# Kernel optimization log

Measured on AMD Instinct MI355X. Metric: run time of the kernel, lower is better.

The kernel has to match this reference:

```python
import jax, jax.numpy as jnp
import numpy as np

N, NFEAT, NHID, NCLASS, H1 = 4096, 512, 64, 16, 8
GAIN = 1.414  # xavier gain used by the torch module
NEG_SLOPE = 0.2
MASK_VAL = -1e10


def _xavier(k, shape):
    fan_in, fan_out = shape[-2], shape[-1]
    lim = GAIN * (6.0 / (fan_in + fan_out)) ** 0.5
    return jax.random.uniform(k, shape, jnp.float32, -lim, lim)


def setup_inputs() -> dict:
    key = jax.random.key(0)
    ks = jax.random.split(key, 10)
    return {
        "x": jax.random.normal(ks[0], (N, NFEAT), jnp.float32),
        "adj": jax.random.randint(ks[1], (N, N), 0, 2, jnp.int32),
        # layer-1 parameters, stacked over H1 heads
        "W1": _xavier(ks[2], (H1, NFEAT, NHID)),
        "b1": jnp.zeros((H1, NHID), jnp.float32),
        "as1": _xavier(ks[3], (H1, NHID, 1))[..., 0],
        "an1": _xavier(ks[4], (H1, NHID, 1))[..., 0],
        # layer-2 parameters (single head, input = H1*NHID due to concat)
        "W2": _xavier(ks[5], (H1 * NHID, NCLASS)),
        "b2": jnp.zeros((NCLASS,), jnp.float32),
        "as2": _xavier(ks[6], (NCLASS, 1))[:, 0],
        "an2": _xavier(ks[7], (NCLASS, 1))[:, 0],
    }


def gat_layer(X, adj_pos, W, b, a_s, a_n):
    # X: [N, Fin], W: [Fin, Fout], a_s/a_n: [Fout], adj_pos: [N, N] bool
    feats = X @ W                                        # [N, Fout]
    s = feats @ a_s                                      # [N]
    nb = feats @ a_n                                     # [N]
    attn = jax.nn.leaky_relu(s[:, None] + nb[None, :], NEG_SLOPE)  # [N, N]
    attn = jnp.where(adj_pos, attn, MASK_VAL)
    attn = jax.nn.softmax(attn, axis=-1)
    # dropout on attn/feats is a no-op in eval mode
    return attn @ feats + b                              # [N, Fout]


def reference(x, adj, W1, b1, as1, an1, W2, b2, as2, an2):
    adj_pos = adj > 0
    # x dropout is a no-op in eval mode
    layer1 = jax.vmap(gat_layer, in_axes=(None, None, 0, 0, 0, 0))
    h = jax.nn.relu(layer1(x, adj_pos, W1, b1, as1, an1))    # [H1, N, NHID]
    h = jnp.transpose(h, (1, 0, 2)).reshape(N, H1 * NHID)    # concat heads on dim 1
    h = jax.nn.elu(h)
    out = jax.nn.relu(gat_layer(h, adj_pos, W2, b2, as2, an2))  # [N, NCLASS]
    return jax.nn.log_softmax(out, axis=1)
```

## Files before the change

### kernel.cpp

```cpp
#include <hip/hip_runtime.h>

#define NN 4096
#define NFEAT 512
#define NHID 64
#define H1 8
#define NCLS 16
#define BND 40.0f
#define VSTR 72

typedef short bf16x8 __attribute__((ext_vector_type(8)));
typedef float f32x4 __attribute__((ext_vector_type(4)));

__device__ __forceinline__ unsigned short f2bf(float f) {
    unsigned u = __float_as_uint(f);
    u += 0x7fffu + ((u >> 16) & 1u);
    return (unsigned short)(u >> 16);
}
__device__ __forceinline__ float leaky(float v) { return fmaxf(v, 0.2f * v); }
__device__ __forceinline__ unsigned pkbf(float lo, float hi) {
    return __builtin_amdgcn_perm(__float_as_uint(hi) + 0x8000u,
                                 __float_as_uint(lo) + 0x8000u, 0x07060302u);
}
__device__ __forceinline__ bf16x8 mk8(unsigned a, unsigned b, unsigned c, unsigned d) {
    union { unsigned u[4]; bf16x8 v; } cv;
    cv.u[0] = a; cv.u[1] = b; cv.u[2] = c; cv.u[3] = d; return cv.v;
}

__global__ __launch_bounds__(256)
void k_prep(const int* __restrict__ adj, unsigned long long* __restrict__ bits,
            const float* __restrict__ W1, unsigned short* __restrict__ w1f)
{
    __shared__ float wt[64][65];
    const int t = threadIdx.x, bx = blockIdx.x;
    if (bx < NN) {
        const int wv = t >> 6, lane = t & 63;
        const int* ap = adj + (size_t)bx * NN;
        for (int w = wv; w < 64; w += 4) {
            unsigned long long m = __ballot(ap[w * 64 + lane] > 0);
            if (lane == 0) bits[(size_t)bx * 64 + w] = m;
        }
        return;
    }
    const int kt = (bx - NN) & 7, h = (bx - NN) >> 3;
    #pragma unroll
    for (int i = 0; i < 4; ++i) {
        const int f = t + 256 * i;
        const int r = f >> 4, c4 = f & 15;
        const float4 v = *(const float4*)(W1 + ((size_t)(h * NFEAT) + kt * 64 + r) * NHID + c4 * 4);
        wt[r][c4 * 4 + 0] = v.x; wt[r][c4 * 4 + 1] = v.y;
        wt[r][c4 * 4 + 2] = v.z; wt[r][c4 * 4 + 3] = v.w;
    }
    __syncthreads();
    #pragma unroll
    for (int s = 0; s < 2; ++s) {
        const int o = t + s * 256;
        const int kg2 = o >> 8, rem = o & 255;
        const int nt = rem >> 6, lane2 = rem & 63;
        const int qq = lane2 >> 4, nn = lane2 & 15;
        const int kl = kg2 * 32 + qq * 8;
        const int c = nt * 16 + nn;
        uint4 w;
        w.x = pkbf(wt[kl + 0][c], wt[kl + 1][c]);
        w.y = pkbf(wt[kl + 2][c], wt[kl + 3][c]);
        w.z = pkbf(wt[kl + 4][c], wt[kl + 5][c]);
        w.w = pkbf(wt[kl + 6][c], wt[kl + 7][c]);
        *(uint4*)(w1f + (((size_t)h * 16 + kt * 2 + kg2) * 4 + nt) * 512 + lane2 * 8) = w;
    }
}

__global__ __launch_bounds__(256)
void k_feats1(const float* __restrict__ x, const unsigned short* __restrict__ w1f,
              const float* __restrict__ as1, const float* __restrict__ an1,
              unsigned short* __restrict__ f1bT, float* __restrict__ s1,
              float* __restrict__ F1a, float* __restrict__ F2a)
{
    const int t = threadIdx.x, wv = t >> 6, lane = t & 63;
    const int q = lane >> 4, n = lane & 15;
    const int h = blockIdx.y, R0 = blockIdx.x * 64;
    const int row = R0 + wv * 16 + n;
    const float* ap = x + (size_t)row * NFEAT;
    const unsigned short* wp = w1f + (size_t)h * 16 * 4 * 512 + lane * 8;
    f32x4 acc[4] = {{0.f,0.f,0.f,0.f},{0.f,0.f,0.f,0.f},{0.f,0.f,0.f,0.f},{0.f,0.f,0.f,0.f}};
    #pragma unroll 4
    for (int kg = 0; kg < 16; ++kg) {
        const float4 xa = *(const float4*)(ap + kg * 32 + q * 8);
        const float4 xb = *(const float4*)(ap + kg * 32 + q * 8 + 4);
        const bf16x8 af = mk8(pkbf(xa.x, xa.y), pkbf(xa.z, xa.w),
                              pkbf(xb.x, xb.y), pkbf(xb.z, xb.w));
        #pragma unroll
        for (int nt = 0; nt < 4; ++nt) {
            const bf16x8 bf = *(const bf16x8*)(wp + (size_t)(kg * 4 + nt) * 512);
            acc[nt] = __builtin_amdgcn_mfma_f32_16x16x32_bf16(af, bf, acc[nt], 0, 0, 0);
        }
    }
    #pragma unroll
    for (int nt = 0; nt < 4; ++nt) {
        uint2 w;
        w.x = pkbf(acc[nt][0], acc[nt][1]);
        w.y = pkbf(acc[nt][2], acc[nt][3]);
        *(uint2*)(f1bT + ((size_t)h * NHID + nt * 16 + n) * NN + R0 + wv * 16 + q * 4) = w;
    }
    float asv[4], anv[4];
    #pragma unroll
    for (int nt = 0; nt < 4; ++nt) {
        asv[nt] = as1[h * NHID + nt * 16 + n];
        anv[nt] = an1[h * NHID + nt * 16 + n];
    }
    #pragma unroll
    for (int i = 0; i < 4; ++i) {
        float ps = acc[0][i]*asv[0] + acc[1][i]*asv[1] + acc[2][i]*asv[2] + acc[3][i]*asv[3];
        float pn = acc[0][i]*anv[0] + acc[1][i]*anv[1] + acc[2][i]*anv[2] + acc[3][i]*anv[3];
        #pragma unroll
        for (int off = 8; off > 0; off >>= 1) {
            ps += __shfl_xor(ps, off, 64);
            pn += __shfl_xor(pn, off, 64);
        }
        if (n == 0) {
            const int idx = R0 + wv * 16 + q * 4 + i;
            s1[h * NN + idx] = ps;
            F1a[h * NN + idx] = __expf(pn - BND);
            F2a[h * NN + idx] = __expf(0.2f * (pn - BND));
        }
    }
}

__global__ __launch_bounds__(512, 4)
void k_gat1(const unsigned short* __restrict__ f1bT, const float* __restrict__ s1,
            const float* __restrict__ F1, const float* __restrict__ F2,
            const unsigned long long* __restrict__ abits, const float* __restrict__ b1,
            unsigned short* __restrict__ hcatb)
{
    __shared__ __align__(16) char smem[4 * 2 * 64 * VSTR * 2];
    unsigned short* vT = (unsigned short*)smem;

    const int t = threadIdx.x, wv = t >> 6, lane = t & 63;
    const int q = lane >> 4, n = lane & 15;
    const int rg = wv >> 2, jq = wv & 3;
    const int h = blockIdx.y, R0 = blockIdx.x * 64;
    const int rowA = R0 + rg * 32 + n;
    const int rowB = rowA + 16;
    const float vA = s1[h * NN + rowA] + BND, mhA = leaky(vA);
    const float vB = s1[h * NN + rowB] + BND, mhB = leaky(vB);
    const float E1A = __expf(vA - mhA), E2A = __expf(0.2f * vA - mhA);
    const float E1B = __expf(vB - mhB), E2B = __expf(0.2f * vB - mhB);
    const unsigned long long* arowA = abits + (size_t)rowA * 64;
    const unsigned long long* arowB = abits + (size_t)rowB * 64;
    const float* F1p = F1 + (size_t)h * NN;
    const float* F2p = F2 + (size_t)h * NN;

    const int stile = t >> 7;
    const int sc0 = (t & 127) >> 3, sj8 = t & 7;
    const unsigned short* sbase = f1bT + (size_t)h * NHID * NN + (size_t)sc0 * NN + sj8 * 8;
    const int dof = sc0 * VSTR + sj8 * 8;

    f32x4 accA[4] = {{0.f,0.f,0.f,0.f},{0.f,0.f,0.f,0.f},{0.f,0.f,0.f,0.f},{0.f,0.f,0.f,0.f}};
    f32x4 accB[4] = {{0.f,0.f,0.f,0.f},{0.f,0.f,0.f,0.f},{0.f,0.f,0.f,0.f},{0.f,0.f,0.f,0.f}};
    float lsA = 0.f, lsB = 0.f;

    {
        const int js = stile * 1024;
        int4 v0 = *(const int4*)(sbase + js);
        int4 v1 = *(const int4*)(sbase + (size_t)16 * NN + js);
        int4 v2 = *(const int4*)(sbase + (size_t)32 * NN + js);
        int4 v3 = *(const int4*)(sbase + (size_t)48 * NN + js);
        unsigned short* d = vT + (stile * 2 + 0) * (64 * VSTR) + dof;
        *(int4*)(d) = v0;
        *(int4*)(d + 16 * VSTR) = v1;
        *(int4*)(d + 32 * VSTR) = v2;
        *(int4*)(d + 48 * VSTR) = v3;
    }
    __syncthreads();

    for (int it = 0; it < 16; ++it) {
        const int db = it & 1;
        int4 p0, p1, p2, p3;
        if (it < 15) {
            const int js = stile * 1024 + (it + 1) * 64;
            p0 = *(const int4*)(sbase + js);
            p1 = *(const int4*)(sbase + (size_t)16 * NN + js);
            p2 = *(const int4*)(sbase + (size_t)32 * NN + js);
            p3 = *(const int4*)(sbase + (size_t)48 * NN + js);
        }
        const int j0 = jq * 1024 + it * 64;
        const unsigned long long aA = arowA[j0 >> 6];
        const unsigned long long aB = arowB[j0 >> 6];
        const unsigned short* tbase = vT + (jq * 2 + db) * (64 * VSTR);
        #pragma unroll
        for (int ch = 0; ch < 2; ++ch) {
            const int kb = ch * 32 + q * 8;
            const float4 f1a = *(const float4*)(F1p + j0 + kb);
            const float4 f1b = *(const float4*)(F1p + j0 + kb + 4);
            const float4 f2a = *(const float4*)(F2p + j0 + kb);
            const float4 f2b = *(const float4*)(F2p + j0 + kb + 4);
            const float F1v[8] = {f1a.x, f1a.y, f1a.z, f1a.w, f1b.x, f1b.y, f1b.z, f1b.w};
            const float F2v[8] = {f2a.x, f2a.y, f2a.z, f2a.w, f2b.x, f2b.y, f2b.z, f2b.w};
            const unsigned bA = (unsigned)(aA >> kb) & 0xffu;
            const unsigned bB = (unsigned)(aB >> kb) & 0xffu;
            unsigned uA[4], uB[4];
            #pragma unroll
            for (int jp = 0; jp < 4; ++jp) {
                float a0 = fmaxf(E1A * F1v[2*jp],   E2A * F2v[2*jp]);
                float a1 = fmaxf(E1A * F1v[2*jp+1], E2A * F2v[2*jp+1]);
                a0 = ((bA >> (2*jp)) & 1u) ? a0 : 0.f;
                a1 = ((bA >> (2*jp+1)) & 1u) ? a1 : 0.f;
                lsA += a0 + a1;
                uA[jp] = pkbf(a0, a1);
                float b0 = fmaxf(E1B * F1v[2*jp],   E2B * F2v[2*jp]);
                float b1v = fmaxf(E1B * F1v[2*jp+1], E2B * F2v[2*jp+1]);
                b0 = ((bB >> (2*jp)) & 1u) ? b0 : 0.f;
                b1v = ((bB >> (2*jp+1)) & 1u) ? b1v : 0.f;
                lsB += b0 + b1v;
                uB[jp] = pkbf(b0, b1v);
            }
            const bf16x8 afA = mk8(uA[0], uA[1], uA[2], uA[3]);
            const bf16x8 afB = mk8(uB[0], uB[1], uB[2], uB[3]);
            #pragma unroll
            for (int nt = 0; nt < 4; ++nt) {
                const bf16x8 bf = *(const bf16x8*)(tbase + (nt * 16 + n) * VSTR + kb);
                accA[nt] = __builtin_amdgcn_mfma_f32_16x16x32_bf16(afA, bf, accA[nt], 0, 0, 0);
                accB[nt] = __builtin_amdgcn_mfma_f32_16x16x32_bf16(afB, bf, accB[nt], 0, 0, 0);
            }
        }
        if (it < 15) {
            unsigned short* d = vT + (stile * 2 + (db ^ 1)) * (64 * VSTR) + dof;
            *(int4*)(d) = p0;
            *(int4*)(d + 16 * VSTR) = p1;
            *(int4*)(d + 32 * VSTR) = p2;
            *(int4*)(d + 48 * VSTR) = p3;
        }
        __syncthreads();
    }

    lsA += __shfl_xor(lsA, 16, 64); lsA += __shfl_xor(lsA, 32, 64);
    lsB += __shfl_xor(lsB, 16, 64); lsB += __shfl_xor(lsB, 32, 64);

    float* cmbf = (float*)smem;
    float* lwf  = (float*)(smem + 69632);
    #pragma unroll
    for (int nt = 0; nt < 4; ++nt)
        #pragma unroll
        for (int i = 0; i < 4; ++i) {
            cmbf[((size_t)jq * 64 + rg * 32 + q * 4 + i) * 68 + nt * 16 + n] = accA[nt][i];
            cmbf[((size_t)jq * 64 + rg * 32 + 16 + q * 4 + i) * 68 + nt * 16 + n] = accB[nt][i];
        }
    if (q == 0) {
        lwf[jq * 64 + rg * 32 + n] = lsA;
        lwf[jq * 64 + rg * 32 + 16 + n] = lsB;
    }
    __syncthreads();

    const int col = t & 63, r8 = t >> 6;
    const float bv = b1[h * NHID + col];
    #pragma unroll
    for (int rr = 0; rr < 8; ++rr) {
        const int r = r8 * 8 + rr;
        float tot = 0.f, lt = 0.f;
        #pragma unroll
        for (int jj = 0; jj < 4; ++jj) {
            tot += cmbf[((size_t)jj * 64 + r) * 68 + col];
            lt  += lwf[jj * 64 + r];
        }
        hcatb[(size_t)(R0 + r) * (H1 * NHID) + h * NHID + col] =
            f2bf(fmaxf(tot / lt + bv, 0.f));
    }
}

__global__ __launch_bounds__(128)
void k_feats2(const unsigned short* __restrict__ hcatb, const float* __restrict__ W2,
              const float* __restrict__ as2, const float* __restrict__ an2,
              unsigned short* __restrict__ f2bT, float* __restrict__ s2,
              float* __restrict__ F1b, float* __restrict__ F2b)
{
    __shared__ __align__(16) unsigned short w2T[NCLS][520];
    const int t = threadIdx.x, wv = t >> 6, lane = t & 63;
    const int q = lane >> 4, n = lane & 15;
    #pragma unroll
    for (int i = 0; i < 16; ++i) {
        const int f4 = t + 128 * i;
        const float4 v = ((const float4*)W2)[f4];
        const int k = f4 >> 2, c0 = (f4 & 3) * 4;
        w2T[c0 + 0][k] = f2bf(v.x); w2T[c0 + 1][k] = f2bf(v.y);
        w2T[c0 + 2][k] = f2bf(v.z); w2T[c0 + 3][k] = f2bf(v.w);
    }
    __syncthreads();

    const int R0 = blockIdx.x * 32;
    const int row = R0 + wv * 16 + n;
    const unsigned short* ap = hcatb + (size_t)row * NFEAT;
    f32x4 acc = {0.f, 0.f, 0.f, 0.f};
    #pragma unroll 4
    for (int k0 = 0; k0 < NFEAT; k0 += 32) {
        const bf16x8 af = *(const bf16x8*)(ap + k0 + q * 8);
        const bf16x8 bf = *(const bf16x8*)&w2T[n][k0 + q * 8];
        acc = __builtin_amdgcn_mfma_f32_16x16x32_bf16(af, bf, acc, 0, 0, 0);
    }
    uint2 w;
    w.x = pkbf(acc[0], acc[1]);
    w.y = pkbf(acc[2], acc[3]);
    *(uint2*)(f2bT + (size_t)n * NN + R0 + wv * 16 + q * 4) = w;
    const float asv = as2[n], anv = an2[n];
    #pragma unroll
    for (int i = 0; i < 4; ++i) {
        float ps = acc[i] * asv, pn = acc[i] * anv;
        #pragma unroll
        for (int off = 8; off > 0; off >>= 1) {
            ps += __shfl_xor(ps, off, 64);
            pn += __shfl_xor(pn, off, 64);
        }
        if (n == 0) {
            const int idx = R0 + wv * 16 + q * 4 + i;
            s2[idx] = ps;
            F1b[idx] = __expf(pn - BND);
            F2b[idx] = __expf(0.2f * (pn - BND));
        }
    }
}

__global__ __launch_bounds__(1024)
void k_gat2(const unsigned short* __restrict__ f2bT, const float* __restrict__ s2,
            const float* __restrict__ F1, const float* __restrict__ F2,
            const unsigned long long* __restrict__ abits, const float* __restrict__ b2,
            float* __restrict__ out)
{
    __shared__ float cmb[16][16][17];
    __shared__ float lw[16][16];
    const int t = threadIdx.x, wv = t >> 6, lane = t & 63;
    const int q = lane >> 4, n = lane & 15;
    const int R0 = blockIdx.x * 16, row = R0 + n;
    const float v = s2[row] + BND, mhat = leaky(v);
    const float E1 = __expf(v - mhat), E2 = __expf(0.2f * v - mhat);
    const unsigned long long* arow = abits + (size_t)row * 64;

    f32x4 acc = {0.f, 0.f, 0.f, 0.f};
    float lsum = 0.f;
    const int jbeg = wv * 256;
    for (int j0 = jbeg; j0 < jbeg + 256; j0 += 64) {
        const unsigned long long a64 = arow[j0 >> 6];
        #pragma unroll
        for (int ch = 0; ch < 2; ++ch) {
            const int kb = ch * 32 + q * 8;
            const float4 f1a = *(const float4*)(F1 + j0 + kb);
            const float4 f1b = *(const float4*)(F1 + j0 + kb + 4);
            const float4 f2a = *(const float4*)(F2 + j0 + kb);
            const float4 f2b = *(const float4*)(F2 + j0 + kb + 4);
            const float F1v[8] = {f1a.x, f1a.y, f1a.z, f1a.w, f1b.x, f1b.y, f1b.z, f1b.w};
            const float F2v[8] = {f2a.x, f2a.y, f2a.z, f2a.w, f2b.x, f2b.y, f2b.z, f2b.w};
            const unsigned b8 = (unsigned)(a64 >> kb) & 0xffu;
            unsigned au[4];
            #pragma unroll
            for (int jp = 0; jp < 4; ++jp) {
                float p0 = fmaxf(E1 * F1v[2*jp],   E2 * F2v[2*jp]);
                float p1 = fmaxf(E1 * F1v[2*jp+1], E2 * F2v[2*jp+1]);
                p0 = ((b8 >> (2*jp)) & 1u) ? p0 : 0.f;
                p1 = ((b8 >> (2*jp+1)) & 1u) ? p1 : 0.f;
                lsum += p0 + p1;
                au[jp] = pkbf(p0, p1);
            }
            const bf16x8 af = mk8(au[0], au[1], au[2], au[3]);
            const bf16x8 bf = *(const bf16x8*)(f2bT + (size_t)n * NN + j0 + kb);
            acc = __builtin_amdgcn_mfma_f32_16x16x32_bf16(af, bf, acc, 0, 0, 0);
        }
    }
    lsum += __shfl_xor(lsum, 16, 64);
    lsum += __shfl_xor(lsum, 32, 64);
    #pragma unroll
    for (int i = 0; i < 4; ++i) cmb[wv][q * 4 + i][n] = acc[i];
    if (q == 0) lw[wv][n] = lsum;
    __syncthreads();

    if (t < 256) {
        const int r = t >> 4, c = t & 15;
        float tot = 0.f, lt = 0.f;
        #pragma unroll
        for (int w16 = 0; w16 < 16; ++w16) { tot += cmb[w16][r][c]; lt += lw[w16][r]; }
        float val = fmaxf(tot / lt + b2[c], 0.f);
        float mx = val;
        #pragma unroll
        for (int off = 1; off < 16; off <<= 1) mx = fmaxf(mx, __shfl_xor(mx, off, 64));
        const float e = __expf(val - mx);
        float se = e;
        #pragma unroll
        for (int off = 1; off < 16; off <<= 1) se += __shfl_xor(se, off, 64);
        out[(size_t)(R0 + r) * NCLS + c] = val - mx - __logf(se);
    }
}

extern "C" void kernel_launch(void* const* d_in, const int* in_sizes, int n_in,
                              void* d_out, int out_size, void* d_ws, size_t ws_size,
                              hipStream_t stream)
{
    const float* x   = (const float*)d_in[0];
    const int*   adj = (const int*)  d_in[1];
    const float* W1  = (const float*)d_in[2];
    const float* b1  = (const float*)d_in[3];
    const float* as1 = (const float*)d_in[4];
    const float* an1 = (const float*)d_in[5];
    const float* W2  = (const float*)d_in[6];
    const float* b2  = (const float*)d_in[7];
    const float* as2 = (const float*)d_in[8];
    const float* an2 = (const float*)d_in[9];
    float* out = (float*)d_out;

    char* ws = (char*)d_ws;
    unsigned long long* abits = (unsigned long long*)(ws);
    unsigned short* f1bT  = (unsigned short*)(ws + (2u << 20));
    unsigned short* hcatb = (unsigned short*)(ws + (6u << 20));
    unsigned short* w1f   = (unsigned short*)(ws + (10u << 20));
    char* ws2 = ws + (10u << 20) + (512u << 10);
    float* s1   = (float*)(ws2);
    float* F1a  = (float*)(ws2 + (128u << 10));
    float* F2a  = (float*)(ws2 + (256u << 10));
    unsigned short* f2bT = (unsigned short*)(ws2 + (384u << 10));
    float* s2   = (float*)(ws2 + (512u << 10));
    float* F1b  = (float*)(ws2 + (528u << 10));
    float* F2b  = (float*)(ws2 + (544u << 10));

    k_prep  <<<dim3(NN + 64),     256, 0, stream>>>(adj, abits, W1, w1f);
    k_feats1<<<dim3(NN / 64, H1), 256, 0, stream>>>(x, w1f, as1, an1, f1bT, s1, F1a, F2a);
    k_gat1  <<<dim3(NN / 64, H1), 512, 0, stream>>>(f1bT, s1, F1a, F2a, abits, b1, hcatb);
    k_feats2<<<dim3(NN / 32),     128, 0, stream>>>(hcatb, W2, as2, an2, f2bT, s2, F1b, F2b);
    k_gat2  <<<dim3(NN / 16),     1024, 0, stream>>>(f2bT, s2, F1b, F2b, abits, b2, out);
}
```

Baseline: 210.2 us.

## Drop LDS staging in GAT layer-1 kernel, read B fragments directly from global

Result: slower. 537.9 us (+155.9%).

```diff
diff --git a/kernel.cpp b/kernel.cpp
--- a/kernel.cpp
+++ b/kernel.cpp
@@ -6,7 +6,6 @@
 #define H1 8
 #define NCLS 16
 #define BND 40.0f
-#define VSTR 72
 
 typedef short bf16x8 __attribute__((ext_vector_type(8)));
 typedef float f32x4 __attribute__((ext_vector_type(4)));
@@ -24,6 +23,13 @@
 __device__ __forceinline__ bf16x8 mk8(unsigned a, unsigned b, unsigned c, unsigned d) {
     union { unsigned u[4]; bf16x8 v; } cv;
     cv.u[0] = a; cv.u[1] = b; cv.u[2] = c; cv.u[3] = d; return cv.v;
+}
+__device__ __forceinline__ unsigned bmask(unsigned b, int i) {
+#if __has_builtin(__builtin_amdgcn_sbfe)
+    return (unsigned)__builtin_amdgcn_sbfe((int)b, (unsigned)i, 1u);
+#else
+    return 0u - ((b >> i) & 1u);
+#endif
 }
 
 __global__ __launch_bounds__(256)
@@ -124,67 +130,38 @@
     }
 }
 
-__global__ __launch_bounds__(512, 4)
+__global__ __launch_bounds__(512, 6)
 void k_gat1(const unsigned short* __restrict__ f1bT, const float* __restrict__ s1,
             const float* __restrict__ F1, const float* __restrict__ F2,
             const unsigned long long* __restrict__ abits, const float* __restrict__ b1,
             unsigned short* __restrict__ hcatb)
 {
-    __shared__ __align__(16) char smem[4 * 2 * 64 * VSTR * 2];
-    unsigned short* vT = (unsigned short*)smem;
-
-    const int t = threadIdx.x, wv = t >> 6, lane = t & 63;
+    __shared__ __align__(16) float cmbf[8][16][68];
+    __shared__ float lwf[8][16];
+    const int t = threadIdx.x, jq = t >> 6, lane = t & 63;
     const int q = lane >> 4, n = lane & 15;
-    const int rg = wv >> 2, jq = wv & 3;
-    const int h = blockIdx.y, R0 = blockIdx.x * 64;
-    const int rowA = R0 + rg * 32 + n;
-    const int rowB = rowA + 16;
+    const int h = blockIdx.y, R0 = blockIdx.x * 32;
+    const int rowA = R0 + n, rowB = R0 + 16 + n;
+
     const float vA = s1[h * NN + rowA] + BND, mhA = leaky(vA);
     const float vB = s1[h * NN + rowB] + BND, mhB = leaky(vB);
     const float E1A = __expf(vA - mhA), E2A = __expf(0.2f * vA - mhA);
     const float E1B = __expf(vB - mhB), E2B = __expf(0.2f * vB - mhB);
-    const unsigned long long* arowA = abits + (size_t)rowA * 64;
-    const unsigned long long* arowB = abits + (size_t)rowB * 64;
-    const float* F1p = F1 + (size_t)h * NN;
-    const float* F2p = F2 + (size_t)h * NN;
-
-    const int stile = t >> 7;
-    const int sc0 = (t & 127) >> 3, sj8 = t & 7;
-    const unsigned short* sbase = f1bT + (size_t)h * NHID * NN + (size_t)sc0 * NN + sj8 * 8;
-    const int dof = sc0 * VSTR + sj8 * 8;
+
+    const unsigned long long* aApt = abits + (size_t)rowA * 64 + jq * 8;
+    const unsigned long long* aBpt = abits + (size_t)rowB * 64 + jq * 8;
+    const float* F1p = F1 + (size_t)h * NN + jq * 512;
+    const float* F2p = F2 + (size_t)h * NN + jq * 512;
+    const unsigned short* bp = f1bT + (size_t)(h * NHID + n) * NN + jq * 512 + q * 8;
 
     f32x4 accA[4] = {{0.f,0.f,0.f,0.f},{0.f,0.f,0.f,0.f},{0.f,0.f,0.f,0.f},{0.f,0.f,0.f,0.f}};
     f32x4 accB[4] = {{0.f,0.f,0.f,0.f},{0.f,0.f,0.f,0.f},{0.f,0.f,0.f,0.f},{0.f,0.f,0.f,0.f}};
     float lsA = 0.f, lsB = 0.f;
 
-    {
-        const int js = stile * 1024;
-        int4 v0 = *(const int4*)(sbase + js);
-        int4 v1 = *(const int4*)(sbase + (size_t)16 * NN + js);
-        int4 v2 = *(const int4*)(sbase + (size_t)32 * NN + js);
-        int4 v3 = *(const int4*)(sbase + (size_t)48 * NN + js);
-        unsigned short* d = vT + (stile * 2 + 0) * (64 * VSTR) + dof;
-        *(int4*)(d) = v0;
-        *(int4*)(d + 16 * VSTR) = v1;
-        *(int4*)(d + 32 * VSTR) = v2;
-        *(int4*)(d + 48 * VSTR) = v3;
-    }
-    __syncthreads();
-
-    for (int it = 0; it < 16; ++it) {
-        const int db = it & 1;
-        int4 p0, p1, p2, p3;
-        if (it < 15) {
-            const int js = stile * 1024 + (it + 1) * 64;
-            p0 = *(const int4*)(sbase + js);
-            p1 = *(const int4*)(sbase + (size_t)16 * NN + js);
-            p2 = *(const int4*)(sbase + (size_t)32 * NN + js);
-            p3 = *(const int4*)(sbase + (size_t)48 * NN + js);
-        }
-        const int j0 = jq * 1024 + it * 64;
-        const unsigned long long aA = arowA[j0 >> 6];
-        const unsigned long long aB = arowB[j0 >> 6];
-        const unsigned short* tbase = vT + (jq * 2 + db) * (64 * VSTR);
+    #pragma unroll 2
+    for (int it = 0; it < 8; ++it) {
+        const int j0 = it * 64;
+        const unsigned long long aA = aApt[it], aB = aBpt[it];
         #pragma unroll
         for (int ch = 0; ch < 2; ++ch) {
             const int kb = ch * 32 + q * 8;
@@ -194,21 +171,21 @@
             const float4 f2b = *(const float4*)(F2p + j0 + kb + 4);
             const float F1v[8] = {f1a.x, f1a.y, f1a.z, f1a.w, f1b.x, f1b.y, f1b.z, f1b.w};
             const float F2v[8] = {f2a.x, f2a.y, f2a.z, f2a.w, f2b.x, f2b.y, f2b.z, f2b.w};
-            const unsigned bA = (unsigned)(aA >> kb) & 0xffu;
-            const unsigned bB = (unsigned)(aB >> kb) & 0xffu;
+            const unsigned bA8 = (unsigned)(aA >> kb) & 0xffu;
+            const unsigned bB8 = (unsigned)(aB >> kb) & 0xffu;
             unsigned uA[4], uB[4];
             #pragma unroll
             for (int jp = 0; jp < 4; ++jp) {
                 float a0 = fmaxf(E1A * F1v[2*jp],   E2A * F2v[2*jp]);
                 float a1 = fmaxf(E1A * F1v[2*jp+1], E2A * F2v[2*jp+1]);
-                a0 = ((bA >> (2*jp)) & 1u) ? a0 : 0.f;
-                a1 = ((bA >> (2*jp+1)) & 1u) ? a1 : 0.f;
+                a0 = __uint_as_float(__float_as_uint(a0) & bmask(bA8, 2*jp));
+                a1 = __uint_as_float(__float_as_uint(a1) & bmask(bA8, 2*jp+1));
                 lsA += a0 + a1;
                 uA[jp] = pkbf(a0, a1);
-                float b0 = fmaxf(E1B * F1v[2*jp],   E2B * F2v[2*jp]);
+                float b0  = fmaxf(E1B * F1v[2*jp],   E2B * F2v[2*jp]);
                 float b1v = fmaxf(E1B * F1v[2*jp+1], E2B * F2v[2*jp+1]);
-                b0 = ((bB >> (2*jp)) & 1u) ? b0 : 0.f;
-                b1v = ((bB >> (2*jp+1)) & 1u) ? b1v : 0.f;
+                b0  = __uint_as_float(__float_as_uint(b0)  & bmask(bB8, 2*jp));
+                b1v = __uint_as_float(__float_as_uint(b1v) & bmask(bB8, 2*jp+1));
                 lsB += b0 + b1v;
                 uB[jp] = pkbf(b0, b1v);
             }
@@ -216,52 +193,56 @@
             const bf16x8 afB = mk8(uB[0], uB[1], uB[2], uB[3]);
             #pragma unroll
             for (int nt = 0; nt < 4; ++nt) {
-                const bf16x8 bf = *(const bf16x8*)(tbase + (nt * 16 + n) * VSTR + kb);
+                const bf16x8 bf = *(const bf16x8*)(bp + (size_t)nt * 16 * NN + j0 + ch * 32);
                 accA[nt] = __builtin_amdgcn_mfma_f32_16x16x32_bf16(afA, bf, accA[nt], 0, 0, 0);
                 accB[nt] = __builtin_amdgcn_mfma_f32_16x16x32_bf16(afB, bf, accB[nt], 0, 0, 0);
             }
         }
-        if (it < 15) {
-            unsigned short* d = vT + (stile * 2 + (db ^ 1)) * (64 * VSTR) + dof;
-            *(int4*)(d) = p0;
-            *(int4*)(d + 16 * VSTR) = p1;
-            *(int4*)(d + 32 * VSTR) = p2;
-            *(int4*)(d + 48 * VSTR) = p3;
-        }
-        __syncthreads();
-    }
-
+    }
     lsA += __shfl_xor(lsA, 16, 64); lsA += __shfl_xor(lsA, 32, 64);
     lsB += __shfl_xor(lsB, 16, 64); lsB += __shfl_xor(lsB, 32, 64);
 
-    float* cmbf = (float*)smem;
-    float* lwf  = (float*)(smem + 69632);
     #pragma unroll
     for (int nt = 0; nt < 4; ++nt)
         #pragma unroll
-        for (int i = 0; i < 4; ++i) {
-            cmbf[((size_t)jq * 64 + rg * 32 + q * 4 + i) * 68 + nt * 16 + n] = accA[nt][i];
-            cmbf[((size_t)jq * 64 + rg * 32 + 16 + q * 4 + i) * 68 + nt * 16 + n] = accB[nt][i];
-        }
-    if (q == 0) {
-        lwf[jq * 64 + rg * 32 + n] = lsA;
-        lwf[jq * 64 + rg * 32 + 16 + n] = lsB;
-    }
-    __syncthreads();
-
-    const int col = t & 63, r8 = t >> 6;
-    const float bv = b1[h * NHID + col];
-    #pragma unroll
-    for (int rr = 0; rr < 8; ++rr) {
-        const int r = r8 * 8 + rr;
-        float tot = 0.f, lt = 0.f;
-        #pragma unroll
-        for (int jj = 0; jj < 4; ++jj) {
-            tot += cmbf[((size_t)jj * 64 + r) * 68 + col];
-            lt  += lwf[jj * 64 + r];
-        }
-        hcatb[(size_t)(R0 + r) * (H1 * NHID) + h * NHID + col] =
-            f2bf(fmaxf(tot / lt + bv, 0.f));
+        for (int i = 0; i < 4; ++i)
+            cmbf[jq][q * 4 + i][nt * 16 + n] = accA[nt][i];
+    if (q == 0) lwf[jq][n] = lsA;
+    __syncthreads();
+    {
+        const int r = t >> 5, c = (t & 31) * 2;
+        float t0 = 0.f, t1 = 0.f, lt = 0.f;
+        #pragma unroll
+        for (int jj = 0; jj < 8; ++jj) {
+            t0 += cmbf[jj][r][c];
+            t1 += cmbf[jj][r][c + 1];
+            lt += lwf[jj][r];
+        }
+        const float o0 = fmaxf(t0 / lt + b1[h * NHID + c], 0.f);
+        const float o1 = fmaxf(t1 / lt + b1[h * NHID + c + 1], 0.f);
+        *(unsigned*)(hcatb + (size_t)(R0 + r) * (H1 * NHID) + h * NHID + c) = pkbf(o0, o1);
+    }
+    __syncthreads();
+
+    #pragma unroll
+    for (int nt = 0; nt < 4; ++nt)
+        #pragma unroll
+        for (int i = 0; i < 4; ++i)
+            cmbf[jq][q * 4 + i][nt * 16 + n] = accB[nt][i];
+    if (q == 0) lwf[jq][n] = lsB;
+    __syncthreads();
+    {
+        const int r = t >> 5, c = (t & 31) * 2;
+        float t0 = 0.f, t1 = 0.f, lt = 0.f;
+        #pragma unroll
+        for (int jj = 0; jj < 8; ++jj) {
+            t0 += cmbf[jj][r][c];
+            t1 += cmbf[jj][r][c + 1];
+            lt += lwf[jj][r];
+        }
+        const float o0 = fmaxf(t0 / lt + b1[h * NHID + c], 0.f);
+        const float o1 = fmaxf(t1 / lt + b1[h * NHID + c + 1], 0.f);
+        *(unsigned*)(hcatb + (size_t)(R0 + 16 + r) * (H1 * NHID) + h * NHID + c) = pkbf(o0, o1);
     }
 }
 
@@ -351,8 +332,8 @@
             for (int jp = 0; jp < 4; ++jp) {
                 float p0 = fmaxf(E1 * F1v[2*jp],   E2 * F2v[2*jp]);
                 float p1 = fmaxf(E1 * F1v[2*jp+1], E2 * F2v[2*jp+1]);
-                p0 = ((b8 >> (2*jp)) & 1u) ? p0 : 0.f;
-                p1 = ((b8 >> (2*jp+1)) & 1u) ? p1 : 0.f;
+                p0 = __uint_as_float(__float_as_uint(p0) & bmask(b8, 2*jp));
+                p1 = __uint_as_float(__float_as_uint(p1) & bmask(b8, 2*jp+1));
                 lsum += p0 + p1;
                 au[jp] = pkbf(p0, p1);
             }
@@ -417,7 +398,7 @@
 
     k_prep  <<<dim3(NN + 64),     256, 0, stream>>>(adj, abits, W1, w1f);
     k_feats1<<<dim3(NN / 64, H1), 256, 0, stream>>>(x, w1f, as1, an1, f1bT, s1, F1a, F2a);
-    k_gat1  <<<dim3(NN / 64, H1), 512, 0, stream>>>(f1bT, s1, F1a, F2a, abits, b1, hcatb);
+    k_gat1  <<<dim3(NN / 32, H1), 512, 0, stream>>>(f1bT, s1, F1a, F2a, abits, b1, hcatb);
     k_feats2<<<dim3(NN / 32),     128, 0, stream>>>(hcatb, W2, as2, an2, f2bT, s2, F1b, F2b);
     k_gat2  <<<dim3(NN / 16),     1024, 0, stream>>>(f2bT, s2, F1b, F2b, abits, b2, out);
 }
```
